# Performance work log

Hardware: AMD Instinct MI355X
Metric: run time of the kernel (lower is better)

## Reference

```python
import jax, jax.numpy as jnp
import numpy as np
import math

B, F, T = 32, 512, 4000
H, DK, DV = 8, 64, 64

def setup_inputs() -> dict:
    key = jax.random.key(0)
    ks = jax.random.split(key, 8)
    x = jax.random.normal(ks[0], (B, F, T), dtype=jnp.float32)
    weights = jax.random.randint(ks[1], (B, T), 0, 2, dtype=jnp.int32)
    # learned params
    q = jax.random.normal(ks[2], (H, DK), dtype=jnp.float32) / math.sqrt(DK)  # (1,H,1,dk) squeezed
    lim_k = 1.0 / math.sqrt(F)
    Wk = jax.random.uniform(ks[3], (H * DK, F), minval=-lim_k, maxval=lim_k, dtype=jnp.float32)
    bk = jax.random.uniform(ks[4], (H * DK,), minval=-lim_k, maxval=lim_k, dtype=jnp.float32)
    Wv = jax.random.uniform(ks[5], (H * DV, F), minval=-lim_k, maxval=lim_k, dtype=jnp.float32)
    bv = jax.random.uniform(ks[6], (H * DV,), minval=-lim_k, maxval=lim_k, dtype=jnp.float32)
    return {"x": x, "weights": weights, "q": q, "Wk": Wk, "bk": bk, "Wv": Wv, "bv": bv}

def reference(x, weights, q, Wk, bk, Wv, bv):
    # x: (B, F, T) -> transpose to (B, T, F) since dim=-1
    xt = jnp.swapaxes(x, 1, 2)                                  # (B,T,F)
    k = (xt @ Wk.T + bk).reshape(B, T, H, DK)                   # (B,T,H,dk)
    v = (xt @ Wv.T + bv).reshape(B, T, H, DV)                   # (B,T,H,dv)
    # scores: q (H,dk) dot k -> (B,H,T), scaled
    scores = jnp.einsum('hd,bthd->bht', q, k) / math.sqrt(DK)
    mask = (weights == 0)[:, None, :]                           # (B,1,T)
    scores = jnp.where(mask, jnp.float32(-1e30), scores)
    attn = jax.nn.softmax(scores, axis=-1)
    attn = jnp.where(mask, 0.0, attn)                           # (B,H,T)
    out = jnp.einsum('bht,bthv->bhv', attn, v)                  # (B,H,dv)
    return out.reshape(B, H * DV)                               # keepdim=False
```

## Files before the change

kernel.cpp:

```cpp
#include <hip/hip_runtime.h>
#include <math.h>

#define BB 32
#define FF 512
#define TT 4000
#define HH 8
#define DKK 64
#define DVV 64
#define NT4 1000

__global__ __launch_bounds__(256) void prep_qk(const float* __restrict__ q,
                                               const float* __restrict__ Wk,
                                               const float* __restrict__ bk,
                                               float* __restrict__ qk,
                                               float* __restrict__ qb) {
    int gid = blockIdx.x * 256 + threadIdx.x;
    int h = gid >> 9, f = gid & 511;
    float s = 0.f;
#pragma unroll 8
    for (int d = 0; d < DKK; ++d)
        s += q[h * DKK + d] * Wk[(size_t)(h * DKK + d) * FF + f];
    qk[gid] = s * 0.125f;
    if (gid < HH) {
        float sb = 0.f;
        for (int d = 0; d < DKK; ++d) sb += q[gid * DKK + d] * bk[gid * DKK + d];
        qb[gid] = sb * 0.125f;
    }
}

__global__ __launch_bounds__(256) void prep_wvt(const float* __restrict__ Wv,
                                                float* __restrict__ WvT) {
    __shared__ float tile[64][65];
    int hv0 = blockIdx.x * 64, f0 = blockIdx.y * 64;
    int tj = threadIdx.x & 63, ti = threadIdx.x >> 6;
#pragma unroll
    for (int r = 0; r < 16; ++r) {
        int i = ti * 16 + r;
        tile[i][tj] = Wv[(size_t)(hv0 + i) * FF + f0 + tj];
    }
    __syncthreads();
#pragma unroll
    for (int r = 0; r < 16; ++r) {
        int i = ti * 16 + r;
        WvT[(size_t)(f0 + i) * FF + hv0 + tj] = tile[tj][i];
    }
}

__global__ __launch_bounds__(256) void k_scores(const float* __restrict__ x,
                                                const float* __restrict__ qk,
                                                const float* __restrict__ qb,
                                                float* __restrict__ sc) {
    __shared__ float4 part[HH * 4 * 64];
    int b = blockIdx.y, tt = blockIdx.x;
    int tid = threadIdx.x, w = tid >> 6, l = tid & 63;
    int t0 = tt << 8;
    int t = t0 + (l << 2);
    float4 acc[HH];
#pragma unroll
    for (int h = 0; h < HH; ++h) acc[h] = make_float4(0.f, 0.f, 0.f, 0.f);
    if (t < TT) {
        const float* xp = x + (size_t)b * FF * TT + t;
        int f40 = w * 32;
#pragma unroll 2
        for (int f4 = f40; f4 < f40 + 32; ++f4) {
            int f = f4 << 2;
            float4 xv0 = *(const float4*)(xp + (size_t)(f + 0) * TT);
            float4 xv1 = *(const float4*)(xp + (size_t)(f + 1) * TT);
            float4 xv2 = *(const float4*)(xp + (size_t)(f + 2) * TT);
            float4 xv3 = *(const float4*)(xp + (size_t)(f + 3) * TT);
#pragma unroll
            for (int h = 0; h < HH; ++h) {
                float4 qv = *(const float4*)(qk + h * FF + f);
                acc[h].x += qv.x * xv0.x + qv.y * xv1.x + qv.z * xv2.x + qv.w * xv3.x;
                acc[h].y += qv.x * xv0.y + qv.y * xv1.y + qv.z * xv2.y + qv.w * xv3.y;
                acc[h].z += qv.x * xv0.z + qv.y * xv1.z + qv.z * xv2.z + qv.w * xv3.z;
                acc[h].w += qv.x * xv0.w + qv.y * xv1.w + qv.z * xv2.w + qv.w * xv3.w;
            }
        }
    }
#pragma unroll
    for (int h = 0; h < HH; ++h) part[(h * 4 + w) * 64 + l] = acc[h];
    __syncthreads();
    for (int p = tid; p < 512; p += 256) {
        int h = p >> 6, ll = p & 63;
        int t2 = t0 + (ll << 2);
        if (t2 >= TT) continue;
        float4 a0 = part[(h * 4 + 0) * 64 + ll];
        float4 a1 = part[(h * 4 + 1) * 64 + ll];
        float4 a2 = part[(h * 4 + 2) * 64 + ll];
        float4 a3 = part[(h * 4 + 3) * 64 + ll];
        float qbh = qb[h];
        float4 o;
        o.x = a0.x + a1.x + a2.x + a3.x + qbh;
        o.y = a0.y + a1.y + a2.y + a3.y + qbh;
        o.z = a0.z + a1.z + a2.z + a3.z + qbh;
        o.w = a0.w + a1.w + a2.w + a3.w + qbh;
        *(float4*)(sc + ((size_t)(b * HH + h)) * TT + t2) = o;
    }
}

__global__ __launch_bounds__(256) void k_softmax(float* __restrict__ sc,
                                                 const int* __restrict__ wts) {
    __shared__ float s4[4];
    int bh = blockIdx.x, b = bh >> 3;
    int tid = threadIdx.x, w = tid >> 6, l = tid & 63;
    float* row = sc + (size_t)bh * TT;
    const int* wr = wts + (size_t)b * TT;
    float4 v[4];
    float m = -3.0e38f;
#pragma unroll
    for (int k = 0; k < 4; ++k) {
        int i = tid + k * 256;
        if (i < NT4) {
            float4 s = *(const float4*)(row + (i << 2));
            int4 wv = *(const int4*)(wr + (i << 2));
            if (wv.x == 0) s.x = -1e30f;
            if (wv.y == 0) s.y = -1e30f;
            if (wv.z == 0) s.z = -1e30f;
            if (wv.w == 0) s.w = -1e30f;
            v[k] = s;
            m = fmaxf(m, fmaxf(fmaxf(s.x, s.y), fmaxf(s.z, s.w)));
        }
    }
#pragma unroll
    for (int d = 1; d < 64; d <<= 1) m = fmaxf(m, __shfl_xor(m, d));
    if (l == 0) s4[w] = m;
    __syncthreads();
    m = fmaxf(fmaxf(s4[0], s4[1]), fmaxf(s4[2], s4[3]));
    __syncthreads();
    float lsum = 0.f;
#pragma unroll
    for (int k = 0; k < 4; ++k) {
        int i = tid + k * 256;
        if (i < NT4) {
            float4 s = v[k];
            s.x = __expf(s.x - m);
            s.y = __expf(s.y - m);
            s.z = __expf(s.z - m);
            s.w = __expf(s.w - m);
            v[k] = s;
            lsum += s.x + s.y + s.z + s.w;
        }
    }
#pragma unroll
    for (int d = 1; d < 64; d <<= 1) lsum += __shfl_xor(lsum, d);
    if (l == 0) s4[w] = lsum;
    __syncthreads();
    lsum = s4[0] + s4[1] + s4[2] + s4[3];
    float inv = (m <= -1e29f) ? 0.f : (1.f / lsum);
#pragma unroll
    for (int k = 0; k < 4; ++k) {
        int i = tid + k * 256;
        if (i < NT4) {
            float4 s = v[k];
            s.x *= inv; s.y *= inv; s.z *= inv; s.w *= inv;
            *(float4*)(row + (i << 2)) = s;
        }
    }
}

__global__ __launch_bounds__(256) void k_y(const float* __restrict__ x,
                                           const float* __restrict__ attn,
                                           float* __restrict__ y) {
    __shared__ float red[32 * 257];
    __shared__ float red2[32 * 8];
    int b = blockIdx.y, ft = blockIdx.x;
    int tid = threadIdx.x;
    int f0 = ft << 2;
    float acc[8][4];
#pragma unroll
    for (int h = 0; h < 8; ++h)
#pragma unroll
        for (int f = 0; f < 4; ++f) acc[h][f] = 0.f;
    const float* ab = attn + (size_t)b * HH * TT;
    const float* xb = x + ((size_t)b * FF + f0) * TT;
    for (int i = tid; i < NT4; i += 256) {
        int t = i << 2;
        float4 a[8];
#pragma unroll
        for (int h = 0; h < 8; ++h) a[h] = *(const float4*)(ab + (size_t)h * TT + t);
        float4 xv[4];
#pragma unroll
        for (int f = 0; f < 4; ++f) xv[f] = *(const float4*)(xb + (size_t)f * TT + t);
#pragma unroll
        for (int h = 0; h < 8; ++h)
#pragma unroll
            for (int f = 0; f < 4; ++f)
                acc[h][f] += a[h].x * xv[f].x + a[h].y * xv[f].y +
                             a[h].z * xv[f].z + a[h].w * xv[f].w;
    }
#pragma unroll
    for (int o = 0; o < 32; ++o) red[o * 257 + tid] = acc[o >> 2][o & 3];
    __syncthreads();
    {
        int o = tid >> 3, seg = tid & 7;
        float s = 0.f;
#pragma unroll
        for (int j = 0; j < 32; ++j) s += red[o * 257 + seg * 32 + j];
        red2[o * 8 + seg] = s;
    }
    __syncthreads();
    if (tid < 32) {
        float vsum = 0.f;
#pragma unroll
        for (int j = 0; j < 8; ++j) vsum += red2[tid * 8 + j];
        int h = tid >> 2, fo = tid & 3;
        y[((size_t)b * HH + h) * FF + f0 + fo] = vsum;
    }
}

__global__ __launch_bounds__(256) void k_out(const float* __restrict__ y,
                                             const float* __restrict__ WvT,
                                             const float* __restrict__ bv,
                                             float* __restrict__ out) {
    __shared__ float ys[4 * FF];
    int half = blockIdx.x, b = blockIdx.y, tid = threadIdx.x;
    int h0 = half * 4;
    const float* yr = y + ((size_t)b * HH + h0) * FF;
    for (int i = tid; i < 4 * FF; i += 256) ys[i] = yr[i];
    __syncthreads();
    int hv = half * 256 + tid;
    int hloc = tid >> 6;
    const float* ysr = ys + hloc * FF;
    float acc = 0.f;
#pragma unroll 8
    for (int f = 0; f < FF; ++f)
        acc += ysr[f] * WvT[(size_t)f * FF + hv];
    out[b * 512 + hv] = acc + bv[hv];
}

extern "C" void kernel_launch(void* const* d_in, const int* in_sizes, int n_in,
                              void* d_out, int out_size, void* d_ws, size_t ws_size,
                              hipStream_t stream) {
    const float* x   = (const float*)d_in[0];
    const int*   wts = (const int*)d_in[1];
    const float* q   = (const float*)d_in[2];
    const float* Wk  = (const float*)d_in[3];
    const float* bk  = (const float*)d_in[4];
    const float* Wv  = (const float*)d_in[5];
    const float* bv  = (const float*)d_in[6];
    float* out = (float*)d_out;
    float* ws  = (float*)d_ws;

    float* qk  = ws;
    float* qb  = ws + 4096;
    float* WvT = ws + 8192;
    float* sc  = ws + 270336;
    float* y   = ws + 1294336;

    prep_qk<<<16, 256, 0, stream>>>(q, Wk, bk, qk, qb);
    prep_wvt<<<dim3(8, 8), 256, 0, stream>>>(Wv, WvT);
    k_scores<<<dim3(16, 32), 256, 0, stream>>>(x, qk, qb, sc);
    k_softmax<<<256, 256, 0, stream>>>(sc, wts);
    k_y<<<dim3(128, 32), 256, 0, stream>>>(x, sc, y);
    k_out<<<dim3(2, 32), 256, 0, stream>>>(y, WvT, bv, out);
}
```

Baseline: 474.2 us.

## Fuse scores, softmax and attention-weighted sum into one flash-style split-T kernel

Replaces the separate score, softmax and weighted-sum kernels with a single kernel. Each block handles one batch and one 512-step time chunk, streaming x tiles into LDS through double-buffered global_load_lds and keeping an online softmax with running max and sum per head. Partial weighted sums per chunk are merged in a combine kernel that also applies the Wv projection. x is now read once instead of twice and the score matrix no longer round-trips through global memory. The cost is only 256 blocks of 512 threads with about 130KB of LDS each, so occupancy and overlap may be low.

Result: faster. 457.2 us (-3.6%).

```diff
diff --git a/kernel.cpp b/kernel.cpp
--- a/kernel.cpp
+++ b/kernel.cpp
@@ -5,9 +5,9 @@
 #define FF 512
 #define TT 4000
 #define HH 8
-#define DKK 64
-#define DVV 64
-#define NT4 1000
+#define NCH 8
+#define CHT 512
+#define TILE 32
 
 __global__ __launch_bounds__(256) void prep_qk(const float* __restrict__ q,
                                                const float* __restrict__ Wk,
@@ -18,12 +18,12 @@
     int h = gid >> 9, f = gid & 511;
     float s = 0.f;
 #pragma unroll 8
-    for (int d = 0; d < DKK; ++d)
-        s += q[h * DKK + d] * Wk[(size_t)(h * DKK + d) * FF + f];
+    for (int d = 0; d < 64; ++d)
+        s += q[h * 64 + d] * Wk[(size_t)(h * 64 + d) * FF + f];
     qk[gid] = s * 0.125f;
     if (gid < HH) {
         float sb = 0.f;
-        for (int d = 0; d < DKK; ++d) sb += q[gid * DKK + d] * bk[gid * DKK + d];
+        for (int d = 0; d < 64; ++d) sb += q[gid * 64 + d] * bk[gid * 64 + d];
         qb[gid] = sb * 0.125f;
     }
 }
@@ -46,187 +46,193 @@
     }
 }
 
-__global__ __launch_bounds__(256) void k_scores(const float* __restrict__ x,
-                                                const float* __restrict__ qk,
-                                                const float* __restrict__ qb,
-                                                float* __restrict__ sc) {
-    __shared__ float4 part[HH * 4 * 64];
-    int b = blockIdx.y, tt = blockIdx.x;
-    int tid = threadIdx.x, w = tid >> 6, l = tid & 63;
-    int t0 = tt << 8;
-    int t = t0 + (l << 2);
-    float4 acc[HH];
-#pragma unroll
-    for (int h = 0; h < HH; ++h) acc[h] = make_float4(0.f, 0.f, 0.f, 0.f);
-    if (t < TT) {
-        const float* xp = x + (size_t)b * FF * TT + t;
-        int f40 = w * 32;
-#pragma unroll 2
-        for (int f4 = f40; f4 < f40 + 32; ++f4) {
-            int f = f4 << 2;
-            float4 xv0 = *(const float4*)(xp + (size_t)(f + 0) * TT);
-            float4 xv1 = *(const float4*)(xp + (size_t)(f + 1) * TT);
-            float4 xv2 = *(const float4*)(xp + (size_t)(f + 2) * TT);
-            float4 xv3 = *(const float4*)(xp + (size_t)(f + 3) * TT);
-#pragma unroll
-            for (int h = 0; h < HH; ++h) {
-                float4 qv = *(const float4*)(qk + h * FF + f);
-                acc[h].x += qv.x * xv0.x + qv.y * xv1.x + qv.z * xv2.x + qv.w * xv3.x;
-                acc[h].y += qv.x * xv0.y + qv.y * xv1.y + qv.z * xv2.y + qv.w * xv3.y;
-                acc[h].z += qv.x * xv0.z + qv.y * xv1.z + qv.z * xv2.z + qv.w * xv3.z;
-                acc[h].w += qv.x * xv0.w + qv.y * xv1.w + qv.z * xv2.w + qv.w * xv3.w;
+#define XS_WORDS (2 * FF * TILE)
+#define PS_OFF   XS_WORDS
+#define AL_OFF   (PS_OFF + HH * TILE)
+#define QB_OFF   (AL_OFF + 8)
+#define LDS_FLOATS (QB_OFF + 8)
+
+extern __shared__ float smem[];
+
+__global__ __launch_bounds__(512) void k_fused(
+    const float* __restrict__ x, const int* __restrict__ wts,
+    const float* __restrict__ qkg, const float* __restrict__ qbg,
+    float* __restrict__ y_part, float* __restrict__ m_part,
+    float* __restrict__ l_part) {
+    float* xs  = smem;
+    float* ps  = smem + PS_OFF;
+    float* al8 = smem + AL_OFF;
+    float* qb8 = smem + QB_OFF;
+
+    const int b = blockIdx.y, ch = blockIdx.x;
+    const int tid = threadIdx.x;
+    const int w = tid >> 6;
+    const int l = tid & 63;
+    const int t4 = l >> 3;
+    const int fs = l & 7;
+    const int f0 = fs * 64;
+    const int h = w;
+    const int tstart = ch * CHT;
+    const int ntile = (ch == NCH - 1) ? 13 : 16;
+
+    if (tid < 8) qb8[tid] = qbg[tid];
+
+    float4 qkr[16];
+#pragma unroll
+    for (int j4 = 0; j4 < 16; ++j4)
+        qkr[j4] = *(const float4*)(qkg + h * FF + f0 + 4 * j4);
+
+    float yacc[8];
+#pragma unroll
+    for (int i = 0; i < 8; ++i) yacc[i] = 0.f;
+    float m_run = -3.0e38f, l_run = 0.f;
+
+    const float* xb = x + (size_t)b * FF * TT;
+    const int* wb = wts + (size_t)b * TT;
+
+#define STAGE(kt, bi, k0, k1)                                                  \
+    {                                                                          \
+        int t0_ = tstart + (kt) * TILE;                                        \
+        _Pragma("unroll")                                                      \
+        for (int k = (k0); k < (k1); ++k) {                                    \
+            int u = k * 512 + tid;                                             \
+            int f_ = u >> 3, t4s = u & 7;                                      \
+            int t4g = t4s ^ (f_ & 7);                                          \
+            const float* g = xb + (size_t)f_ * TT + t0_ + 4 * t4g;             \
+            float* ldst = xs + (bi) * (FF * TILE) + (k * 512 + w * 64) * 4;    \
+            __builtin_amdgcn_global_load_lds(                                  \
+                (const __attribute__((address_space(1))) unsigned int*)g,      \
+                (__attribute__((address_space(3))) unsigned int*)ldst,         \
+                16, 0, 0);                                                     \
+        }                                                                      \
+    }
+
+    STAGE(0, 0, 0, 8);
+    __syncthreads();
+
+    for (int kt = 0; kt < ntile; ++kt) {
+        int cur = kt & 1, nxt = cur ^ 1;
+        if (kt + 1 < ntile) STAGE(kt + 1, nxt, 0, 4);
+
+        int tglob = tstart + kt * TILE + 4 * t4;
+        int4 w4 = *(const int4*)(wb + tglob);
+        const float* xcur = xs + cur * (FF * TILE);
+        float4 s4 = make_float4(0.f, 0.f, 0.f, 0.f);
+#pragma unroll
+        for (int j4 = 0; j4 < 16; ++j4) {
+            int f = f0 + 4 * j4;
+            float4 qv = qkr[j4];
+            float4 x0 = *(const float4*)(xcur + (f + 0) * TILE + 4 * (t4 ^ ((f + 0) & 7)));
+            float4 x1 = *(const float4*)(xcur + (f + 1) * TILE + 4 * (t4 ^ ((f + 1) & 7)));
+            float4 x2 = *(const float4*)(xcur + (f + 2) * TILE + 4 * (t4 ^ ((f + 2) & 7)));
+            float4 x3 = *(const float4*)(xcur + (f + 3) * TILE + 4 * (t4 ^ ((f + 3) & 7)));
+            s4.x += qv.x * x0.x + qv.y * x1.x + qv.z * x2.x + qv.w * x3.x;
+            s4.y += qv.x * x0.y + qv.y * x1.y + qv.z * x2.y + qv.w * x3.y;
+            s4.z += qv.x * x0.z + qv.y * x1.z + qv.z * x2.z + qv.w * x3.z;
+            s4.w += qv.x * x0.w + qv.y * x1.w + qv.z * x2.w + qv.w * x3.w;
+        }
+#pragma unroll
+        for (int mk = 1; mk <= 4; mk <<= 1) {
+            s4.x += __shfl_xor(s4.x, mk);
+            s4.y += __shfl_xor(s4.y, mk);
+            s4.z += __shfl_xor(s4.z, mk);
+            s4.w += __shfl_xor(s4.w, mk);
+        }
+        float qbh = qb8[h];
+        float sm0 = w4.x ? (s4.x + qbh) : -1e30f;
+        float sm1 = w4.y ? (s4.y + qbh) : -1e30f;
+        float sm2 = w4.z ? (s4.z + qbh) : -1e30f;
+        float sm3 = w4.w ? (s4.w + qbh) : -1e30f;
+        float tm = fmaxf(fmaxf(sm0, sm1), fmaxf(sm2, sm3));
+#pragma unroll
+        for (int mk = 8; mk <= 32; mk <<= 1) tm = fmaxf(tm, __shfl_xor(tm, mk));
+        float nm = fmaxf(m_run, tm);
+        float al = __expf(m_run - nm);
+        float e0 = w4.x ? __expf(sm0 - nm) : 0.f;
+        float e1 = w4.y ? __expf(sm1 - nm) : 0.f;
+        float e2 = w4.z ? __expf(sm2 - nm) : 0.f;
+        float e3 = w4.w ? __expf(sm3 - nm) : 0.f;
+        float ts = e0 + e1 + e2 + e3;
+#pragma unroll
+        for (int mk = 8; mk <= 32; mk <<= 1) ts += __shfl_xor(ts, mk);
+        l_run = al * l_run + ts;
+        m_run = nm;
+        if (fs == 0) *(float4*)(ps + h * TILE + 4 * t4) = make_float4(e0, e1, e2, e3);
+        if (l == 0) al8[h] = al;
+
+        __syncthreads();
+
+        if (kt + 1 < ntile) STAGE(kt + 1, nxt, 4, 8);
+
+#pragma unroll
+        for (int hh = 0; hh < 8; ++hh) yacc[hh] *= al8[hh];
+        const float* xrow = xcur + tid * TILE;
+        int fx = tid & 7;
+#pragma unroll
+        for (int g = 0; g < 8; ++g) {
+            float4 xv = *(const float4*)(xrow + 4 * (g ^ fx));
+#pragma unroll
+            for (int hh = 0; hh < 8; ++hh) {
+                float4 e4 = *(const float4*)(ps + hh * TILE + 4 * g);
+                yacc[hh] += e4.x * xv.x + e4.y * xv.y + e4.z * xv.z + e4.w * xv.w;
             }
         }
-    }
-#pragma unroll
-    for (int h = 0; h < HH; ++h) part[(h * 4 + w) * 64 + l] = acc[h];
-    __syncthreads();
-    for (int p = tid; p < 512; p += 256) {
-        int h = p >> 6, ll = p & 63;
-        int t2 = t0 + (ll << 2);
-        if (t2 >= TT) continue;
-        float4 a0 = part[(h * 4 + 0) * 64 + ll];
-        float4 a1 = part[(h * 4 + 1) * 64 + ll];
-        float4 a2 = part[(h * 4 + 2) * 64 + ll];
-        float4 a3 = part[(h * 4 + 3) * 64 + ll];
-        float qbh = qb[h];
-        float4 o;
-        o.x = a0.x + a1.x + a2.x + a3.x + qbh;
-        o.y = a0.y + a1.y + a2.y + a3.y + qbh;
-        o.z = a0.z + a1.z + a2.z + a3.z + qbh;
-        o.w = a0.w + a1.w + a2.w + a3.w + qbh;
-        *(float4*)(sc + ((size_t)(b * HH + h)) * TT + t2) = o;
-    }
-}
-
-__global__ __launch_bounds__(256) void k_softmax(float* __restrict__ sc,
-                                                 const int* __restrict__ wts) {
-    __shared__ float s4[4];
-    int bh = blockIdx.x, b = bh >> 3;
-    int tid = threadIdx.x, w = tid >> 6, l = tid & 63;
-    float* row = sc + (size_t)bh * TT;
-    const int* wr = wts + (size_t)b * TT;
-    float4 v[4];
-    float m = -3.0e38f;
-#pragma unroll
-    for (int k = 0; k < 4; ++k) {
-        int i = tid + k * 256;
-        if (i < NT4) {
-            float4 s = *(const float4*)(row + (i << 2));
-            int4 wv = *(const int4*)(wr + (i << 2));
-            if (wv.x == 0) s.x = -1e30f;
-            if (wv.y == 0) s.y = -1e30f;
-            if (wv.z == 0) s.z = -1e30f;
-            if (wv.w == 0) s.w = -1e30f;
-            v[k] = s;
-            m = fmaxf(m, fmaxf(fmaxf(s.x, s.y), fmaxf(s.z, s.w)));
-        }
-    }
-#pragma unroll
-    for (int d = 1; d < 64; d <<= 1) m = fmaxf(m, __shfl_xor(m, d));
-    if (l == 0) s4[w] = m;
-    __syncthreads();
-    m = fmaxf(fmaxf(s4[0], s4[1]), fmaxf(s4[2], s4[3]));
-    __syncthreads();
-    float lsum = 0.f;
-#pragma unroll
-    for (int k = 0; k < 4; ++k) {
-        int i = tid + k * 256;
-        if (i < NT4) {
-            float4 s = v[k];
-            s.x = __expf(s.x - m);
-            s.y = __expf(s.y - m);
-            s.z = __expf(s.z - m);
-            s.w = __expf(s.w - m);
-            v[k] = s;
-            lsum += s.x + s.y + s.z + s.w;
-        }
-    }
-#pragma unroll
-    for (int d = 1; d < 64; d <<= 1) lsum += __shfl_xor(lsum, d);
-    if (l == 0) s4[w] = lsum;
-    __syncthreads();
-    lsum = s4[0] + s4[1] + s4[2] + s4[3];
-    float inv = (m <= -1e29f) ? 0.f : (1.f / lsum);
-#pragma unroll
-    for (int k = 0; k < 4; ++k) {
-        int i = tid + k * 256;
-        if (i < NT4) {
-            float4 s = v[k];
-            s.x *= inv; s.y *= inv; s.z *= inv; s.w *= inv;
-            *(float4*)(row + (i << 2)) = s;
-        }
-    }
-}
-
-__global__ __launch_bounds__(256) void k_y(const float* __restrict__ x,
-                                           const float* __restrict__ attn,
-                                           float* __restrict__ y) {
-    __shared__ float red[32 * 257];
-    __shared__ float red2[32 * 8];
-    int b = blockIdx.y, ft = blockIdx.x;
-    int tid = threadIdx.x;
-    int f0 = ft << 2;
-    float acc[8][4];
-#pragma unroll
-    for (int h = 0; h < 8; ++h)
-#pragma unroll
-        for (int f = 0; f < 4; ++f) acc[h][f] = 0.f;
-    const float* ab = attn + (size_t)b * HH * TT;
-    const float* xb = x + ((size_t)b * FF + f0) * TT;
-    for (int i = tid; i < NT4; i += 256) {
-        int t = i << 2;
-        float4 a[8];
-#pragma unroll
-        for (int h = 0; h < 8; ++h) a[h] = *(const float4*)(ab + (size_t)h * TT + t);
-        float4 xv[4];
-#pragma unroll
-        for (int f = 0; f < 4; ++f) xv[f] = *(const float4*)(xb + (size_t)f * TT + t);
-#pragma unroll
-        for (int h = 0; h < 8; ++h)
-#pragma unroll
-            for (int f = 0; f < 4; ++f)
-                acc[h][f] += a[h].x * xv[f].x + a[h].y * xv[f].y +
-                             a[h].z * xv[f].z + a[h].w * xv[f].w;
-    }
-#pragma unroll
-    for (int o = 0; o < 32; ++o) red[o * 257 + tid] = acc[o >> 2][o & 3];
-    __syncthreads();
-    {
-        int o = tid >> 3, seg = tid & 7;
-        float s = 0.f;
-#pragma unroll
-        for (int j = 0; j < 32; ++j) s += red[o * 257 + seg * 32 + j];
-        red2[o * 8 + seg] = s;
-    }
-    __syncthreads();
-    if (tid < 32) {
-        float vsum = 0.f;
-#pragma unroll
-        for (int j = 0; j < 8; ++j) vsum += red2[tid * 8 + j];
-        int h = tid >> 2, fo = tid & 3;
-        y[((size_t)b * HH + h) * FF + f0 + fo] = vsum;
-    }
-}
-
-__global__ __launch_bounds__(256) void k_out(const float* __restrict__ y,
-                                             const float* __restrict__ WvT,
-                                             const float* __restrict__ bv,
-                                             float* __restrict__ out) {
-    __shared__ float ys[4 * FF];
+        __syncthreads();
+    }
+
+#pragma unroll
+    for (int hh = 0; hh < 8; ++hh)
+        y_part[(((size_t)b * NCH + ch) * HH + hh) * FF + tid] = yacc[hh];
+    if (l == 0) {
+        m_part[(b * NCH + ch) * HH + h] = m_run;
+        l_part[(b * NCH + ch) * HH + h] = l_run;
+    }
+}
+
+__global__ __launch_bounds__(256) void k_combine_out(
+    const float* __restrict__ y_part, const float* __restrict__ m_part,
+    const float* __restrict__ l_part, const float* __restrict__ WvT,
+    const float* __restrict__ bv, float* __restrict__ out) {
+    __shared__ float ys[4][512];
+    __shared__ float wj[4][NCH];
+    __shared__ float invL[4], bsc[4];
     int half = blockIdx.x, b = blockIdx.y, tid = threadIdx.x;
     int h0 = half * 4;
-    const float* yr = y + ((size_t)b * HH + h0) * FF;
-    for (int i = tid; i < 4 * FF; i += 256) ys[i] = yr[i];
+    if (tid < 32) {
+        int hl = tid >> 3, j = tid & 7;
+        float m = m_part[(b * NCH + j) * HH + h0 + hl];
+        float lv = l_part[(b * NCH + j) * HH + h0 + hl];
+        float M = m;
+#pragma unroll
+        for (int mk = 1; mk <= 4; mk <<= 1) M = fmaxf(M, __shfl_xor(M, mk, 8));
+        float a = __expf(m - M);
+        float L = a * lv;
+#pragma unroll
+        for (int mk = 1; mk <= 4; mk <<= 1) L += __shfl_xor(L, mk, 8);
+        wj[hl][j] = a;
+        if (j == 0) {
+            invL[hl] = (L > 0.f) ? 1.f / L : 0.f;
+            bsc[hl] = (L > 0.f) ? 1.f : 0.f;
+        }
+    }
+    __syncthreads();
+    for (int i = tid; i < 2048; i += 256) {
+        int hl = i >> 9, f = i & 511;
+        float s = 0.f;
+#pragma unroll
+        for (int j = 0; j < NCH; ++j)
+            s += wj[hl][j] * y_part[(((size_t)b * NCH + j) * HH + h0 + hl) * FF + f];
+        ys[hl][f] = s * invL[hl];
+    }
     __syncthreads();
     int hv = half * 256 + tid;
     int hloc = tid >> 6;
-    const float* ysr = ys + hloc * FF;
+    const float* ysr = ys[hloc];
     float acc = 0.f;
 #pragma unroll 8
     for (int f = 0; f < FF; ++f)
         acc += ysr[f] * WvT[(size_t)f * FF + hv];
-    out[b * 512 + hv] = acc + bv[hv];
+    out[b * 512 + hv] = acc + bv[hv] * bsc[hloc];
 }
 
 extern "C" void kernel_launch(void* const* d_in, const int* in_sizes, int n_in,
@@ -242,16 +248,23 @@
     float* out = (float*)d_out;
     float* ws  = (float*)d_ws;
 
-    float* qk  = ws;
-    float* qb  = ws + 4096;
-    float* WvT = ws + 8192;
-    float* sc  = ws + 270336;
-    float* y   = ws + 1294336;
+    float* qk     = ws;
+    float* qb     = ws + 4096;
+    float* WvT    = ws + 8192;
+    float* y_part = ws + 270336;
+    float* m_part = ws + 1318912;
+    float* l_part = ws + 1320960;
 
     prep_qk<<<16, 256, 0, stream>>>(q, Wk, bk, qk, qb);
     prep_wvt<<<dim3(8, 8), 256, 0, stream>>>(Wv, WvT);
-    k_scores<<<dim3(16, 32), 256, 0, stream>>>(x, qk, qb, sc);
-    k_softmax<<<256, 256, 0, stream>>>(sc, wts);
-    k_y<<<dim3(128, 32), 256, 0, stream>>>(x, sc, y);
-    k_out<<<dim3(2, 32), 256, 0, stream>>>(y, WvT, bv, out);
-}
+
+    size_t lds_bytes = (size_t)LDS_FLOATS * 4;
+    (void)hipFuncSetAttribute((const void*)k_fused,
+                              hipFuncAttributeMaxDynamicSharedMemorySize,
+                              (int)lds_bytes);
+    k_fused<<<dim3(NCH, BB), 512, lds_bytes, stream>>>(
+        x, wts, qk, qb, y_part, m_part, l_part);
+
+    k_combine_out<<<dim3(2, BB), 256, 0, stream>>>(
+        y_part, m_part, l_part, WvT, bv, out);
+}
```
